# Optimization experiments

Hardware: AMD Instinct MI355X
Metric: run time of the kernel (lower is better)

## Reference

```python
import jax, jax.numpy as jnp
import numpy as np

B, T, H = 2, 2048, 1024
NH = 16
HD = H // NH


def setup_inputs() -> dict:
    key = jax.random.key(0)
    ks = jax.random.split(key, 9)
    s = 0.02
    return {
        "x": jax.random.normal(ks[0], (B, T, H), dtype=jnp.float32),
        "attn_mask": jnp.ones((B, T), dtype=jnp.int32),
        "Wq": jax.random.normal(ks[1], (H, H), dtype=jnp.float32) * s,
        "bq": jnp.zeros((H,), dtype=jnp.float32),
        "Wk": jax.random.normal(ks[2], (H, H), dtype=jnp.float32) * s,
        "bk": jnp.zeros((H,), dtype=jnp.float32),
        "Wv": jax.random.normal(ks[3], (H, H), dtype=jnp.float32) * s,
        "bv": jnp.zeros((H,), dtype=jnp.float32),
        "Wo": jax.random.normal(ks[4], (H, H), dtype=jnp.float32) * s,
        "bo": jnp.zeros((H,), dtype=jnp.float32),
    }


def reference(x, attn_mask, Wq, bq, Wk, bk, Wv, bv, Wo, bo):
    Bc, Tc, Hc = x.shape
    scale = HD ** -0.5
    # projections; torch Linear: y = x @ W.T + b (here W stored as [in,out])
    q = (x @ Wq + bq).reshape(Bc, Tc, NH, HD).transpose(0, 2, 1, 3)  # [B,NH,T,HD]
    k = (x @ Wk + bk).reshape(Bc, Tc, NH, HD).transpose(0, 2, 1, 3)
    v = (x @ Wv + bv).reshape(Bc, Tc, NH, HD).transpose(0, 2, 1, 3)
    scores = jnp.einsum('bhqd,bhkd->bhqk', q, k) * scale  # [B,NH,T,T]
    mask = attn_mask.reshape(Bc, 1, 1, Tc)
    scores = jnp.where(mask == 0, jnp.float32(-jnp.inf), scores)
    probs = jax.nn.softmax(scores, axis=-1)
    ctx = jnp.einsum('bhqk,bhkd->bhqd', probs, v)  # [B,NH,T,HD]
    ctx = ctx.transpose(0, 2, 1, 3).reshape(Bc, Tc, Hc)
    out = ctx @ Wo + bo
    return out
```

## Files before the change

kernel.cpp:

```cpp
#include <hip/hip_runtime.h>

typedef _Float16 f16;
typedef _Float16 f16x8 __attribute__((ext_vector_type(8)));
typedef _Float16 f16x4 __attribute__((ext_vector_type(4)));
typedef __fp16 h16x2 __attribute__((ext_vector_type(2)));
typedef float f32x4 __attribute__((ext_vector_type(4)));

#define MFMA32(a, b, c) __builtin_amdgcn_mfma_f32_16x16x32_f16((a), (b), (c), 0, 0, 0)
#define MFMA16(a, b, c) __builtin_amdgcn_mfma_f32_16x16x16f16((a), (b), (c), 0, 0, 0)

static constexpr int Bb = 2, T = 2048, H = 1024, NH = 16, HD = 64;
static constexpr int M = Bb * T;
static constexpr int NQKV = 3 * H;
#define QSCALE 0.1803368801111f

__device__ __forceinline__ void gload_lds16(const void* g, void* l) {
  __builtin_amdgcn_global_load_lds(
      (const __attribute__((address_space(1))) void*)g,
      (__attribute__((address_space(3))) void*)l, 16, 0, 0);
}

__global__ __launch_bounds__(256) void pack_all(const float* __restrict__ x,
                                                const float* __restrict__ Wq,
                                                const float* __restrict__ Wk,
                                                const float* __restrict__ Wv,
                                                const float* __restrict__ Wo,
                                                const float* __restrict__ bq,
                                                const float* __restrict__ bk,
                                                const float* __restrict__ bv,
                                                f16* __restrict__ xh,
                                                f16* __restrict__ WqkvT,
                                                f16* __restrict__ WoT,
                                                float* __restrict__ bqkv) {
  __shared__ f16 tile[64][65];
  const int bid = blockIdx.x;
  if (bid < 4096) {
    int i = bid * 256 + threadIdx.x;
    float4 v = ((const float4*)x)[i];
    f16x4 o;
    o[0] = (f16)v.x; o[1] = (f16)v.y; o[2] = (f16)v.z; o[3] = (f16)v.w;
    *(f16x4*)(xh + (size_t)i * 4) = o;
  } else if (bid < 5120) {
    int t = bid - 4096;
    int z = t >> 8, rem = t & 255;
    const float* W = (z == 0) ? Wq : (z == 1) ? Wk : (z == 2) ? Wv : Wo;
    f16* Wt = (z < 3) ? (WqkvT + (size_t)z * H * H) : WoT;
    const float scale = (z == 0) ? QSCALE : 1.0f;
    int k0 = (rem >> 4) * 64, n0 = (rem & 15) * 64;
    for (int p = 0; p < 16; ++p) {
      int idx = threadIdx.x + p * 256;
      int r = idx >> 6, c = idx & 63;
      tile[r][c] = (f16)(W[(size_t)(k0 + r) * H + n0 + c] * scale);
    }
    __syncthreads();
    for (int p = 0; p < 16; ++p) {
      int idx = threadIdx.x + p * 256;
      int r = idx >> 6, c = idx & 63;
      Wt[(size_t)(n0 + r) * H + k0 + c] = tile[c][r];
    }
  } else {
    int i = (bid - 5120) * 256 + threadIdx.x;
    if (i < 3072) {
      float v = (i < 1024) ? bq[i] * QSCALE : ((i < 2048) ? bk[i - 1024] : bv[i - 2048]);
      bqkv[i] = v;
    }
  }
}

__device__ __forceinline__ f16x8 lds_frag(const f16* base, int row, int gr) {
  return *(const f16x8*)(base + row * 64 + ((gr ^ (row & 7)) << 3));
}

template <int TM, int TN, bool OUT_F32>
__global__ __launch_bounds__(256) void gemm_f16_bt(const f16* __restrict__ A,
                                                   const f16* __restrict__ Bt,
                                                   const float* __restrict__ bias,
                                                   void* __restrict__ Cout,
                                                   int Nn, int Kk) {
  __shared__ f16 As[TM * 64];
  __shared__ f16 Bs[TN * 64];
  const int tid = threadIdx.x;
  const int lane = tid & 63, w = tid >> 6;
  const int quad = lane >> 4, l16 = lane & 15;
  const int wm = w >> 1, wn = w & 1;
  const int m0 = blockIdx.y * TM, n0 = blockIdx.x * TN;
  constexpr int AM = TM / 32, AN = TN / 32;

  f32x4 acc[AM][AN];
  for (int a = 0; a < AM; ++a)
    for (int b2 = 0; b2 < AN; ++b2)
      for (int r = 0; r < 4; ++r) acc[a][b2][r] = 0.f;

  for (int k0 = 0; k0 < Kk; k0 += 64) {
    for (int p = 0; p < TM * 8 / 256; ++p) {
      int slot = p * 256 + w * 64 + lane;
      int r = slot >> 3, g = (slot & 7) ^ (r & 7);
      gload_lds16(A + (size_t)(m0 + r) * Kk + k0 + g * 8,
                  (char*)As + (p * 256 + w * 64) * 16);
    }
    for (int p = 0; p < TN * 8 / 256; ++p) {
      int slot = p * 256 + w * 64 + lane;
      int r = slot >> 3, g = (slot & 7) ^ (r & 7);
      gload_lds16(Bt + (size_t)(n0 + r) * Kk + k0 + g * 8,
                  (char*)Bs + (p * 256 + w * 64) * 16);
    }
    __syncthreads();
    for (int ks = 0; ks < 2; ++ks) {
      f16x8 af[AM], bf[AN];
      for (int t = 0; t < AM; ++t)
        af[t] = lds_frag(As, wm * (TM / 2) + t * 16 + l16, ks * 4 + quad);
      for (int t = 0; t < AN; ++t)
        bf[t] = lds_frag(Bs, wn * (TN / 2) + t * 16 + l16, ks * 4 + quad);
      for (int tm = 0; tm < AM; ++tm)
        for (int tn = 0; tn < AN; ++tn)
          acc[tm][tn] = MFMA32(af[tm], bf[tn], acc[tm][tn]);
    }
    __syncthreads();
  }

  for (int tm = 0; tm < AM; ++tm)
    for (int tn = 0; tn < AN; ++tn)
      for (int r = 0; r < 4; ++r) {
        int m = m0 + wm * (TM / 2) + tm * 16 + quad * 4 + r;
        int n = n0 + wn * (TN / 2) + tn * 16 + l16;
        float v = acc[tm][tn][r] + bias[n];
        if (OUT_F32)
          ((float*)Cout)[(size_t)m * Nn + n] = v;
        else
          ((f16*)Cout)[(size_t)m * Nn + n] = (f16)v;
      }
}


__global__ __launch_bounds__(256, 1) void attn_fused(const f16* __restrict__ QKV,
                                                     const int* __restrict__ mask,
                                                     f16* __restrict__ ctx) {
  __shared__ f16 Kt[2][128 * 64];
  __shared__ f16 Vt[2][80 * 128];

  const int tid = threadIdx.x;
  const int w = tid >> 6, lane = tid & 63;
  const int quad = lane >> 4, l16 = lane & 15;
  const int q0 = blockIdx.x * 256, h = blockIdx.y, b = blockIdx.z;

  const int vkv = tid & 127;
  const int vgb = (tid >> 7) * 4;
  const size_t kbase = (size_t)(b * T) * NQKV + H + h * HD;
  const size_t vbase = (size_t)(b * T) * NQKV + 2 * H + h * HD;

  f16x8 qf[4][2];
  for (int tq = 0; tq < 4; ++tq) {
    const f16* qrow = QKV + (size_t)(b * T + q0 + w * 64 + tq * 16 + l16) * NQKV + h * HD;
    qf[tq][0] = *(const f16x8*)(qrow + quad * 8);
    qf[tq][1] = *(const f16x8*)(qrow + 32 + quad * 8);
  }

  f32x4 oacc[4][5];
  for (int tq = 0; tq < 4; ++tq)
    for (int t = 0; t < 5; ++t)
      for (int r = 0; r < 4; ++r) oacc[tq][t][r] = 0.f;

  for (int p = 0; p < 4; ++p) {
    int slot = p * 256 + w * 64 + lane;
    int r = slot >> 3, g = (slot & 7) ^ (r & 7);
    gload_lds16(QKV + kbase + (size_t)r * NQKV + g * 8,
                (char*)&Kt[0][0] + (p * 256 + w * 64) * 16);
  }
  {
    f16 vm = (f16)(float)(mask[b * T + vkv] != 0);
    const f16* vrow = QKV + vbase + (size_t)vkv * NQKV;
    for (int p = 0; p < 4; ++p) {
      int g = vgb + p;
      f16x8 v = *(const f16x8*)(vrow + g * 8);
      for (int j = 0; j < 8; ++j) {
        int d = g * 8 + j;
        Vt[0][d * 128 + ((vkv + 4 * (d & 15)) & 127)] = v[j] * vm;
      }
    }
    if (tid < 128) Vt[0][64 * 128 + vkv] = vm;
  }
  __syncthreads();

  for (int it = 0; it < T / 128; ++it) {
    const int cur = it & 1, nxt = cur ^ 1;
    const int kvn = (it + 1) * 128;
    const bool pf = kvn < T;

    f16x8 vreg[4] = {};
    f16 vm = (f16)0;
    if (pf) {
      for (int p = 0; p < 4; ++p) {
        int slot = p * 256 + w * 64 + lane;
        int r = slot >> 3, g = (slot & 7) ^ (r & 7);
        gload_lds16(QKV + kbase + (size_t)(kvn + r) * NQKV + g * 8,
                    (char*)&Kt[nxt][0] + (p * 256 + w * 64) * 16);
      }
      vm = (f16)(float)(mask[b * T + kvn + vkv] != 0);
      const f16* vrow = QKV + vbase + (size_t)(kvn + vkv) * NQKV;
      for (int p = 0; p < 4; ++p)
        vreg[p] = *(const f16x8*)(vrow + (vgb + p) * 8);
    }

    const f16* Kc = &Kt[cur][0];
    const f16* Vc = &Vt[cur][0];
    for (int tk = 0; tk < 8; ++tk) {
      f16x8 kf0 = lds_frag(Kc, tk * 16 + l16, quad);
      f16x8 kf1 = lds_frag(Kc, tk * 16 + l16, 4 + quad);
      f16x4 vf[5];
      for (int td = 0; td < 5; ++td)
        vf[td] = *(const f16x4*)&Vc[(td * 16 + l16) * 128 +
                                    ((tk * 16 + quad * 4 + 4 * l16) & 127)];
      for (int tq = 0; tq < 4; ++tq) {
        f32x4 s = {0.f, 0.f, 0.f, 0.f};
        s = MFMA32(kf0, qf[tq][0], s);
        s = MFMA32(kf1, qf[tq][1], s);
        h16x2 p01 = __builtin_amdgcn_cvt_pkrtz(__builtin_amdgcn_exp2f(s[0]),
                                               __builtin_amdgcn_exp2f(s[1]));
        h16x2 p23 = __builtin_amdgcn_cvt_pkrtz(__builtin_amdgcn_exp2f(s[2]),
                                               __builtin_amdgcn_exp2f(s[3]));
        f16x4 pfr;
        pfr[0] = (f16)p01[0]; pfr[1] = (f16)p01[1];
        pfr[2] = (f16)p23[0]; pfr[3] = (f16)p23[1];
        for (int td = 0; td < 5; ++td)
          oacc[tq][td] = MFMA16(vf[td], pfr, oacc[tq][td]);
      }
    }

    if (pf) {
      for (int p = 0; p < 4; ++p) {
        int g = vgb + p;
        for (int j = 0; j < 8; ++j) {
          int d = g * 8 + j;
          Vt[nxt][d * 128 + (((kvn + vkv) + 4 * (d & 15)) & 127)] = vreg[p][j] * vm;
        }
      }
      if (tid < 128) Vt[nxt][64 * 128 + vkv] = vm;
      __syncthreads();
    }
  }

  for (int tq = 0; tq < 4; ++tq) {
    float lq = __shfl(oacc[tq][4][0], l16, 64);
    float inv = 1.f / lq;
    int row = b * T + q0 + w * 64 + tq * 16 + l16;
    for (int td = 0; td < 4; ++td) {
      f16x4 o;
      for (int r = 0; r < 4; ++r) o[r] = (f16)(oacc[tq][td][r] * inv);
      *(f16x4*)(ctx + (size_t)row * H + h * HD + td * 16 + quad * 4) = o;
    }
  }
}


extern "C" void kernel_launch(void* const* d_in, const int* in_sizes, int n_in,
                              void* d_out, int out_size, void* d_ws, size_t ws_size,
                              hipStream_t stream) {
  const float* x  = (const float*)d_in[0];
  const int* mask = (const int*)d_in[1];
  const float* Wq = (const float*)d_in[2];
  const float* bq = (const float*)d_in[3];
  const float* Wk = (const float*)d_in[4];
  const float* bk = (const float*)d_in[5];
  const float* Wv = (const float*)d_in[6];
  const float* bv = (const float*)d_in[7];
  const float* Wo = (const float*)d_in[8];
  const float* bo = (const float*)d_in[9];
  float* out = (float*)d_out;

  char* ws = (char*)d_ws;
  f16* xh      = (f16*)(ws);
  f16* Wqkv_t  = (f16*)(ws + (8u  << 20));
  f16* Wot     = (f16*)(ws + (14u << 20));
  float* bqkv  = (float*)(ws + (16u << 20));
  f16* QKV     = (f16*)(ws + (17u << 20));
  f16* ctx     = (f16*)(ws + (42u << 20));

  pack_all<<<dim3(5132), 256, 0, stream>>>(x, Wq, Wk, Wv, Wo, bq, bk, bv,
                                           xh, Wqkv_t, Wot, bqkv);

  gemm_f16_bt<128, 128, false><<<dim3(NQKV / 128, M / 128), 256, 0, stream>>>(
      xh, Wqkv_t, bqkv, QKV, NQKV, H);

  attn_fused<<<dim3(T / 256, NH, Bb), 256, 0, stream>>>(QKV, mask, ctx);

  gemm_f16_bt<128, 64, true><<<dim3(H / 64, M / 128), 256, 0, stream>>>(
      ctx, Wot, bo, out, H, H);
}
```

Baseline: 222.0 us.

## Split attention KV tiles across two wave groups with LDS reduction

```diff
diff --git a/kernel.cpp b/kernel.cpp
--- a/kernel.cpp
+++ b/kernel.cpp
@@ -132,25 +132,31 @@
 }
 
 
-__global__ __launch_bounds__(256, 1) void attn_fused(const f16* __restrict__ QKV,
+static constexpr int KT_ELE = 256 * 64;
+static constexpr int VT_ELE = 66 * 256;
+
+__global__ __launch_bounds__(512, 1) void attn_fused(const f16* __restrict__ QKV,
                                                      const int* __restrict__ mask,
                                                      f16* __restrict__ ctx) {
-  __shared__ f16 Kt[2][128 * 64];
-  __shared__ f16 Vt[2][80 * 128];
+  __shared__ char smem[(2 * KT_ELE + 2 * VT_ELE) * 2];
+  f16* KtB = (f16*)smem;
+  f16* VtB = (f16*)(smem + 2 * KT_ELE * 2);
+  float* cmb = (float*)smem;
 
   const int tid = threadIdx.x;
   const int w = tid >> 6, lane = tid & 63;
   const int quad = lane >> 4, l16 = lane & 15;
+  const int g = w >> 2, wq = w & 3;
   const int q0 = blockIdx.x * 256, h = blockIdx.y, b = blockIdx.z;
 
-  const int vkv = tid & 127;
-  const int vgb = (tid >> 7) * 4;
+  const int vkv = tid & 255;
+  const int vgb = (tid >> 8) * 4;
   const size_t kbase = (size_t)(b * T) * NQKV + H + h * HD;
   const size_t vbase = (size_t)(b * T) * NQKV + 2 * H + h * HD;
 
   f16x8 qf[4][2];
   for (int tq = 0; tq < 4; ++tq) {
-    const f16* qrow = QKV + (size_t)(b * T + q0 + w * 64 + tq * 16 + l16) * NQKV + h * HD;
+    const f16* qrow = QKV + (size_t)(b * T + q0 + wq * 64 + tq * 16 + l16) * NQKV + h * HD;
     qf[tq][0] = *(const f16x8*)(qrow + quad * 8);
     qf[tq][1] = *(const f16x8*)(qrow + 32 + quad * 8);
   }
@@ -161,39 +167,39 @@
       for (int r = 0; r < 4; ++r) oacc[tq][t][r] = 0.f;
 
   for (int p = 0; p < 4; ++p) {
-    int slot = p * 256 + w * 64 + lane;
-    int r = slot >> 3, g = (slot & 7) ^ (r & 7);
-    gload_lds16(QKV + kbase + (size_t)r * NQKV + g * 8,
-                (char*)&Kt[0][0] + (p * 256 + w * 64) * 16);
+    int slot = p * 512 + w * 64 + lane;
+    int r = slot >> 3, gs = (slot & 7) ^ (r & 7);
+    gload_lds16(QKV + kbase + (size_t)r * NQKV + gs * 8,
+                (char*)KtB + (p * 512 + w * 64) * 16);
   }
   {
     f16 vm = (f16)(float)(mask[b * T + vkv] != 0);
     const f16* vrow = QKV + vbase + (size_t)vkv * NQKV;
     for (int p = 0; p < 4; ++p) {
-      int g = vgb + p;
-      f16x8 v = *(const f16x8*)(vrow + g * 8);
+      int gr = vgb + p;
+      f16x8 v = *(const f16x8*)(vrow + gr * 8);
       for (int j = 0; j < 8; ++j) {
-        int d = g * 8 + j;
-        Vt[0][d * 128 + ((vkv + 4 * (d & 15)) & 127)] = v[j] * vm;
-      }
-    }
-    if (tid < 128) Vt[0][64 * 128 + vkv] = vm;
+        int d = gr * 8 + j;
+        VtB[d * 256 + ((vkv + 4 * (d & 15)) & 255)] = v[j] * vm;
+      }
+    }
+    if (tid < 256) VtB[64 * 256 + vkv] = vm;
   }
   __syncthreads();
 
-  for (int it = 0; it < T / 128; ++it) {
+  for (int it = 0; it < T / 256; ++it) {
     const int cur = it & 1, nxt = cur ^ 1;
-    const int kvn = (it + 1) * 128;
+    const int kvn = (it + 1) * 256;
     const bool pf = kvn < T;
 
     f16x8 vreg[4] = {};
     f16 vm = (f16)0;
     if (pf) {
       for (int p = 0; p < 4; ++p) {
-        int slot = p * 256 + w * 64 + lane;
-        int r = slot >> 3, g = (slot & 7) ^ (r & 7);
-        gload_lds16(QKV + kbase + (size_t)(kvn + r) * NQKV + g * 8,
-                    (char*)&Kt[nxt][0] + (p * 256 + w * 64) * 16);
+        int slot = p * 512 + w * 64 + lane;
+        int r = slot >> 3, gs = (slot & 7) ^ (r & 7);
+        gload_lds16(QKV + kbase + (size_t)(kvn + r) * NQKV + gs * 8,
+                    (char*)(KtB + nxt * KT_ELE) + (p * 512 + w * 64) * 16);
       }
       vm = (f16)(float)(mask[b * T + kvn + vkv] != 0);
       const f16* vrow = QKV + vbase + (size_t)(kvn + vkv) * NQKV;
@@ -201,15 +207,15 @@
         vreg[p] = *(const f16x8*)(vrow + (vgb + p) * 8);
     }
 
-    const f16* Kc = &Kt[cur][0];
-    const f16* Vc = &Vt[cur][0];
+    const f16* Kc = KtB + cur * KT_ELE;
+    const f16* Vc = VtB + cur * VT_ELE;
     for (int tk = 0; tk < 8; ++tk) {
-      f16x8 kf0 = lds_frag(Kc, tk * 16 + l16, quad);
-      f16x8 kf1 = lds_frag(Kc, tk * 16 + l16, 4 + quad);
+      f16x8 kf0 = lds_frag(Kc, g * 128 + tk * 16 + l16, quad);
+      f16x8 kf1 = lds_frag(Kc, g * 128 + tk * 16 + l16, 4 + quad);
       f16x4 vf[5];
       for (int td = 0; td < 5; ++td)
-        vf[td] = *(const f16x4*)&Vc[(td * 16 + l16) * 128 +
-                                    ((tk * 16 + quad * 4 + 4 * l16) & 127)];
+        vf[td] = *(const f16x4*)&Vc[(td * 16 + l16) * 256 +
+                                    ((g * 128 + tk * 16 + quad * 4 + 4 * l16) & 255)];
       for (int tq = 0; tq < 4; ++tq) {
         f32x4 s = {0.f, 0.f, 0.f, 0.f};
         s = MFMA32(kf0, qf[tq][0], s);
@@ -227,26 +233,42 @@
     }
 
     if (pf) {
+      f16* Vn = VtB + nxt * VT_ELE;
       for (int p = 0; p < 4; ++p) {
-        int g = vgb + p;
+        int gr = vgb + p;
         for (int j = 0; j < 8; ++j) {
-          int d = g * 8 + j;
-          Vt[nxt][d * 128 + (((kvn + vkv) + 4 * (d & 15)) & 127)] = vreg[p][j] * vm;
+          int d = gr * 8 + j;
+          Vn[d * 256 + ((vkv + 4 * (d & 15)) & 255)] = vreg[p][j] * vm;
         }
       }
-      if (tid < 128) Vt[nxt][64 * 128 + vkv] = vm;
+      if (tid < 256) Vn[64 * 256 + vkv] = vm;
       __syncthreads();
     }
   }
 
-  for (int tq = 0; tq < 4; ++tq) {
-    float lq = __shfl(oacc[tq][4][0], l16, 64);
-    float inv = 1.f / lq;
-    int row = b * T + q0 + w * 64 + tq * 16 + l16;
-    for (int td = 0; td < 4; ++td) {
-      f16x4 o;
-      for (int r = 0; r < 4; ++r) o[r] = (f16)(oacc[tq][td][r] * inv);
-      *(f16x4*)(ctx + (size_t)row * H + h * HD + td * 16 + quad * 4) = o;
+  __syncthreads();
+  if (g == 1) {
+    float* dst = cmb + ((size_t)(wq * 64 + lane)) * 81;
+    for (int tq = 0; tq < 4; ++tq)
+      for (int td = 0; td < 5; ++td)
+        for (int r = 0; r < 4; ++r) dst[(tq * 5 + td) * 4 + r] = oacc[tq][td][r];
+  }
+  __syncthreads();
+  if (g == 0) {
+    const float* src = cmb + ((size_t)(wq * 64 + lane)) * 81;
+    for (int tq = 0; tq < 4; ++tq)
+      for (int td = 0; td < 5; ++td)
+        for (int r = 0; r < 4; ++r) oacc[tq][td][r] += src[(tq * 5 + td) * 4 + r];
+
+    for (int tq = 0; tq < 4; ++tq) {
+      float lq = __shfl(oacc[tq][4][0], l16, 64);
+      float inv = 1.f / lq;
+      int row = b * T + q0 + wq * 64 + tq * 16 + l16;
+      for (int td = 0; td < 4; ++td) {
+        f16x4 o;
+        for (int r = 0; r < 4; ++r) o[r] = (f16)(oacc[tq][td][r] * inv);
+        *(f16x4*)(ctx + (size_t)row * H + h * HD + td * 16 + quad * 4) = o;
+      }
     }
   }
 }
@@ -281,7 +303,7 @@
   gemm_f16_bt<128, 128, false><<<dim3(NQKV / 128, M / 128), 256, 0, stream>>>(
       xh, Wqkv_t, bqkv, QKV, NQKV, H);
 
-  attn_fused<<<dim3(T / 256, NH, Bb), 256, 0, stream>>>(QKV, mask, ctx);
+  attn_fused<<<dim3(T / 256, NH, Bb), 512, 0, stream>>>(QKV, mask, ctx);
 
   gemm_f16_bt<128, 64, true><<<dim3(H / 64, M / 128), 256, 0, stream>>>(
       ctx, Wot, bo, out, H, H);
```

Result: faster. 210.1 us (-5.4%).
